# Kernel tuning notes

Hardware: AMD Instinct MI355X
Metric: run time of the kernel (lower is better)

The kernel has to match this reference:

```python
import jax, jax.numpy as jnp
import numpy as np

NUM_HEADS = 16
ROPE_BASE = 10000.0


def _rotate_half(x):
    x1 = x[..., ::2]
    x2 = x[..., 1::2]
    return jnp.stack((-x2, x1), axis=-1).reshape(x.shape)


def _rope_tables(seq_len, head_dim, dtype):
    inv_freq = 1.0 / (ROPE_BASE ** (jnp.arange(0, head_dim, 2, dtype=jnp.float32) / head_dim))
    t = jnp.arange(seq_len, dtype=jnp.float32)
    freqs = jnp.outer(t, inv_freq)            # [S, head_dim//2]
    emb = jnp.concatenate((freqs, freqs), -1)  # [S, head_dim]
    return jnp.cos(emb).astype(dtype), jnp.sin(emb).astype(dtype)


def setup_inputs() -> dict:
    key = jax.random.key(0)
    ks = jax.random.split(key, 5)
    B, S, H = 1, 4096, 1024
    scale = 1.0 / np.sqrt(H)
    return {
        "x": jax.random.normal(ks[0], (B, S, H), jnp.float32),
        "Wq": jax.random.normal(ks[1], (H, H), jnp.float32) * scale,
        "Wk": jax.random.normal(ks[2], (H, H), jnp.float32) * scale,
        "Wv": jax.random.normal(ks[3], (H, H), jnp.float32) * scale,
        "Wo": jax.random.normal(ks[4], (H, H), jnp.float32) * scale,
        "attention_mask": jnp.ones((B, S), jnp.int32),
    }


def reference(x, Wq, Wk, Wv, Wo, attention_mask):
    B, S, H = x.shape
    hd = H // NUM_HEADS

    def split_heads(t):  # [B,S,H] -> [B,nh,S,hd]
        return t.reshape(B, S, NUM_HEADS, hd).transpose(0, 2, 1, 3)

    q = split_heads(x @ Wq)
    k = split_heads(x @ Wk)
    v = split_heads(x @ Wv)

    cos, sin = _rope_tables(S, hd, x.dtype)
    cos = cos[None, None]  # [1,1,S,hd]
    sin = sin[None, None]
    q = q * cos + _rotate_half(q) * sin
    k = k * cos + _rotate_half(k) * sin

    scores = jnp.einsum("bhqd,bhkd->bhqk", q, k) / jnp.sqrt(jnp.asarray(hd, x.dtype))
    mask = attention_mask.reshape(B, 1, 1, S)
    scores = jnp.where(mask == 0, jnp.finfo(x.dtype).min, scores)
    probs = jax.nn.softmax(scores, axis=-1)
    ctx = jnp.einsum("bhqk,bhkd->bhqd", probs, v)
    ctx = ctx.transpose(0, 2, 1, 3).reshape(B, S, H)
    return ctx @ Wo
```

## Files before the change

kernel.cpp:

```cpp
#include <hip/hip_runtime.h>
#include <cstdint>
#include <cstddef>

#define S_LEN 4096
#define NHEADS 16
#define HD 64
#define HDIM 1024

typedef _Float16 f16x8 __attribute__((ext_vector_type(8)));
typedef _Float16 f16x4 __attribute__((ext_vector_type(4)));
typedef __fp16 h16x2 __attribute__((ext_vector_type(2)));
typedef float f32x4 __attribute__((ext_vector_type(4)));
typedef unsigned char uchar;
typedef unsigned int u32;

__device__ __forceinline__ f32x4 mfma16h(f16x8 a, f16x8 b, f32x4 c) {
    return __builtin_amdgcn_mfma_f32_16x16x32_f16(a, b, c, 0, 0, 0);
}
__device__ __forceinline__ void async16(void* lds, const void* g) {
    __builtin_amdgcn_global_load_lds(
        (const __attribute__((address_space(1))) u32*)g,
        (__attribute__((address_space(3))) u32*)lds, 16, 0, 0);
}
__device__ __forceinline__ float fdot2_(u32 a, u32 b, float c) {
#if __has_builtin(__builtin_amdgcn_fdot2)
    return __builtin_amdgcn_fdot2(__builtin_bit_cast(h16x2, a),
                                  __builtin_bit_cast(h16x2, b), c, false);
#else
    float d;
    asm volatile("v_dot2_f32_f16 %0, %1, %2, %3"
                 : "=v"(d) : "v"(a), "v"(b), "v"(c));
    return d;
#endif
}
__device__ __forceinline__ float dot8(f16x8 p, uint4 f, float acc) {
    uint4 pw = __builtin_bit_cast(uint4, p);
    acc = fdot2_(pw.x, f.x, acc);
    acc = fdot2_(pw.y, f.y, acc);
    acc = fdot2_(pw.z, f.z, acc);
    acc = fdot2_(pw.w, f.w, acc);
    return acc;
}


__global__ __launch_bounds__(256) void pack_x(const float* __restrict__ X,
                                              uchar* __restrict__ P,
                                              const int* __restrict__ M,
                                              _Float16* __restrict__ FM16)
{
    int id = blockIdx.x * 256 + threadIdx.x;
    int m = id >> 7, g = id & 127;
    int kc = g >> 3, b = g & 7;
    float v[8];
    *(float4*)&v[0] = *(const float4*)&X[(size_t)m * HDIM + kc * 64 + b * 8];
    *(float4*)&v[4] = *(const float4*)&X[(size_t)m * HDIM + kc * 64 + b * 8 + 4];
    __align__(16) _Float16 h[8];
    #pragma unroll
    for (int i = 0; i < 8; i++) h[i] = (_Float16)v[i];
    size_t base = ((size_t)(m * 16 + kc)) * 128 + (size_t)((b ^ (m & 7)) * 16);
    *(uint4*)(P + base) = *(const uint4*)h;
    if (id < S_LEN) {
        int c = id >> 7, k128 = id & 127;
        int w = k128 >> 5, k32 = k128 & 31;
        int q = (k32 >> 2) & 3, kt = k32 >> 4, r = k32 & 3;
        FM16[c * 128 + w * 32 + q * 8 + kt * 4 + r] =
            (_Float16)((M[id] == 0) ? 0.0f : 1.0f);
    }
}

__global__ __launch_bounds__(256) void pack_w4(
    const float* __restrict__ W0, const float* __restrict__ W1,
    const float* __restrict__ W2, const float* __restrict__ W3,
    uchar* __restrict__ P)
{
    int id = blockIdx.x * 256 + threadIdx.x;
    int wsel = id >> 17;
    int lid  = id & 131071;
    int g = lid >> 10, n = lid & 1023;
    int kc = g >> 3, b = g & 7;
    const float* W = (wsel == 0) ? W0 : (wsel == 1) ? W1 : (wsel == 2) ? W2 : W3;
    uchar* dst = P + (size_t)wsel * 2097152;
    float v[8];
    #pragma unroll
    for (int j = 0; j < 8; j++)
        v[j] = W[(size_t)(kc * 64 + b * 8 + j) * HDIM + n];
    __align__(16) _Float16 h[8];
    #pragma unroll
    for (int i = 0; i < 8; i++) h[i] = (_Float16)v[i];
    size_t base = ((size_t)(n * 16 + kc)) * 128 + (size_t)((b ^ (n & 7)) * 16);
    *(uint4*)(dst + base) = *(const uint4*)h;
}

__global__ __launch_bounds__(256) void gemm_f16(
    const uchar* __restrict__ Ap, const uchar* __restrict__ Bp,
    float* __restrict__ C, int head_major)
{
    __shared__ __align__(16) uchar AB[65536];
    const int t = threadIdx.x, lane = t & 63, w = t >> 6;
    const int quad = lane >> 4, l15 = lane & 15, x7 = l15 & 7;
    const int m0 = blockIdx.y * 128, n0 = blockIdx.x * 128;
    const int wm = (w >> 1) * 64, wn = (w & 1) * 64;

    f32x4 acc[4][4];
    const f32x4 zero4 = {0.0f, 0.0f, 0.0f, 0.0f};
    #pragma unroll
    for (int mt = 0; mt < 4; mt++)
        #pragma unroll
        for (int nt = 0; nt < 4; nt++) acc[mt][nt] = zero4;

    #pragma unroll
    for (int i = 0; i < 4; i++) {
        int idx = i * 256 + t;
        int row = idx >> 3, blk = idx & 7;
        int ldso = (idx & ~63) * 16;
        async16(AB + ldso,         Ap + ((size_t)((m0 + row) * 16 + 0)) * 128 + blk * 16);
        async16(AB + 16384 + ldso, Bp + ((size_t)((n0 + row) * 16 + 0)) * 128 + blk * 16);
    }

    for (int kc = 0; kc < 16; kc++) {
        uchar* As = AB + (kc & 1) * 32768;
        uchar* Bs = As + 16384;
        __syncthreads();
        if (kc + 1 < 16) {
            uchar* An = AB + ((kc + 1) & 1) * 32768;
            #pragma unroll
            for (int i = 0; i < 4; i++) {
                int idx = i * 256 + t;
                int row = idx >> 3, blk = idx & 7;
                int ldso = (idx & ~63) * 16;
                async16(An + ldso,
                        Ap + ((size_t)((m0 + row) * 16 + kc + 1)) * 128 + blk * 16);
                async16(An + 16384 + ldso,
                        Bp + ((size_t)((n0 + row) * 16 + kc + 1)) * 128 + blk * 16);
            }
        }
        #pragma unroll
        for (int ks = 0; ks < 2; ks++) {
            const int phys = ((ks * 4 + quad) ^ x7) * 16;
            f16x8 ah[4];
            #pragma unroll
            for (int mt = 0; mt < 4; mt++)
                ah[mt] = *(const f16x8*)(As + (size_t)(wm + mt * 16 + l15) * 128 + phys);
            #pragma unroll
            for (int nt = 0; nt < 4; nt++) {
                f16x8 bh = *(const f16x8*)(Bs + (size_t)(wn + nt * 16 + l15) * 128 + phys);
                #pragma unroll
                for (int mt = 0; mt < 4; mt++)
                    acc[mt][nt] = mfma16h(ah[mt], bh, acc[mt][nt]);
            }
        }
    }

    #pragma unroll
    for (int mt = 0; mt < 4; mt++)
        #pragma unroll
        for (int nt = 0; nt < 4; nt++)
            #pragma unroll
            for (int r = 0; r < 4; r++) {
                int m = m0 + wm + mt * 16 + quad * 4 + r;
                int n = n0 + wn + nt * 16 + l15;
                float val = acc[mt][nt][r];
                if (head_major) {
                    int hh = n >> 6, d = n & 63;
                    C[((size_t)hh * S_LEN + m) * HD + d] = val;
                } else {
                    C[(size_t)m * HDIM + n] = val;
                }
            }
}

__global__ __launch_bounds__(256) void rope_pack(const float* __restrict__ QKVf,
                                                 uchar* __restrict__ Qg,
                                                 uchar* __restrict__ Kg)
{
    int id = blockIdx.x * 256 + threadIdx.x;
    int g  = id & 7;
    int s  = (id >> 3) & (S_LEN - 1);
    int hb = id >> 15;
    const float* src = QKVf + (size_t)hb * (S_LEN * HD) + (size_t)s * HD + g * 8;
    float v[8];
    *(float4*)&v[0] = *(const float4*)&src[0];
    *(float4*)&v[4] = *(const float4*)&src[4];

    const float L32 = 13.287712379549449f / 32.0f;
    float out[8];
    #pragma unroll
    for (int u = 0; u < 4; u++) {
        int de = g * 8 + 2 * u;
        float ae = (float)s * __builtin_amdgcn_exp2f(-(float)(de & 31) * L32);
        float ao = (float)s * __builtin_amdgcn_exp2f(-(float)((de + 1) & 31) * L32);
        float ce = __cosf(ae), se = __sinf(ae);
        float co = __cosf(ao), so = __sinf(ao);
        float xe = v[2 * u], xo = v[2 * u + 1];
        out[2 * u]     = xe * ce - xo * se;
        out[2 * u + 1] = xo * co + xe * so;
    }
    const bool isQ = hb < 16;
    const float scale = isQ ? 0.18033688011112042f : 1.0f;
    __align__(16) _Float16 h[8];
    #pragma unroll
    for (int i = 0; i < 8; i++) h[i] = (_Float16)(out[i] * scale);
    uchar* dst = (isQ ? Qg : Kg);
    size_t base = ((size_t)((hb & 15) * S_LEN + s)) * 128 + (size_t)((g ^ (s & 7)) * 16);
    *(uint4*)(dst + base) = *(const uint4*)h;
}

__global__ __launch_bounds__(256) void v_pack(const float* __restrict__ Vf,
                                              const int* __restrict__ M,
                                              uchar* __restrict__ Vg)
{
    int id = blockIdx.x * 256 + threadIdx.x;
    int d    = id & 63;
    int kg   = (id >> 6) & 15;
    int kc2  = (id >> 10) & 31;
    int head = id >> 15;
    __align__(16) _Float16 hv[8];
    #pragma unroll
    for (int j = 0; j < 8; j++) {
        int key = kc2 * 128 + kg * 8 + j;
        float x = Vf[(size_t)head * (S_LEN * HD) + (size_t)key * HD + d];
        hv[j] = (M[key] == 0) ? (_Float16)0.0f : (_Float16)x;
    }
    int wv  = kg >> 2;
    int kgm = kg & 3;
    int kt  = kgm >> 1;
    int qA  = (kgm * 2) & 3;
    int qB  = (kgm * 2 + 1) & 3;
    int slotA = wv * 32 + qA * 8 + kt * 4;
    int slotB = wv * 32 + qB * 8 + kt * 4;
    size_t row = ((size_t)(head * 32 + kc2)) * 16384 + (size_t)d * 256;
    *(ushort4*)(Vg + row + (size_t)(((slotA >> 3) ^ (d & 7)) * 16 + (slotA & 7) * 2))
        = *(const ushort4*)&hv[0];
    *(ushort4*)(Vg + row + (size_t)(((slotB >> 3) ^ (d & 7)) * 16 + (slotB & 7) * 2))
        = *(const ushort4*)&hv[4];
}

#define ISSUE_K(CC)                                                            \
  {                                                                            \
    const uchar* ks_ = kgb + (size_t)(CC) * 16384;                             \
    async16(KB,        ks_ + l16);                                             \
    async16(KB + 1024, ks_ + 1024 + l16);                                      \
    async16(KB + 2048, ks_ + 2048 + l16);                                      \
    async16(KB + 3072, ks_ + 3072 + l16);                                      \
  }
#define ISSUE_V(CC)                                                            \
  {                                                                            \
    const uchar* vs_ = vgb + (size_t)(CC) * 16384;                             \
    async16(VB,        vs_ + voff);                                            \
    async16(VB + 1024, vs_ + 4096 + voff);                                     \
    async16(VB + 2048, vs_ + 8192 + voff);                                     \
    async16(VB + 3072, vs_ + 12288 + voff);                                    \
  }

#define ATTN_STEP(CC, TOPC, MIDC, FLG)                                         \
  {                                                                            \
    asm volatile("s_waitcnt vmcnt(" TOPC ")" ::: "memory");                    \
    const int ph0_ = (quad ^ x7) * 16;                                         \
    const int ph1_ = ((4 + quad) ^ x7) * 16;                                   \
    f16x8 ka_ = *(const f16x8*)(KB + (size_t)l15 * 128 + ph0_);                \
    f16x8 kb_ = *(const f16x8*)(KB + (size_t)(16 + l15) * 128 + ph0_);         \
    f16x8 kc_ = *(const f16x8*)(KB + (size_t)l15 * 128 + ph1_);                \
    f16x8 kd_ = *(const f16x8*)(KB + (size_t)(16 + l15) * 128 + ph1_);         \
    asm volatile("s_waitcnt lgkmcnt(0)" ::: "memory");                         \
    if ((CC) + 1 < 32) ISSUE_K((CC) + 1);                                      \
    f16x8 pb[4];                                                               \
    _Pragma("unroll")                                                          \
    for (int qt = 0; qt < 4; qt++) {                                           \
      f32x4 s0 = mfma16h(ka_, qf[qt][0], zero4);                               \
      s0 = mfma16h(kc_, qf[qt][1], s0);                                        \
      f32x4 s1 = mfma16h(kb_, qf[qt][0], zero4);                               \
      s1 = mfma16h(kd_, qf[qt][1], s1);                                        \
      h16x2 c01 = __builtin_amdgcn_cvt_pkrtz(                                  \
          __builtin_amdgcn_exp2f(s0[0]), __builtin_amdgcn_exp2f(s0[1]));       \
      h16x2 c23 = __builtin_amdgcn_cvt_pkrtz(                                  \
          __builtin_amdgcn_exp2f(s0[2]), __builtin_amdgcn_exp2f(s0[3]));       \
      h16x2 c45 = __builtin_amdgcn_cvt_pkrtz(                                  \
          __builtin_amdgcn_exp2f(s1[0]), __builtin_amdgcn_exp2f(s1[1]));       \
      h16x2 c67 = __builtin_amdgcn_cvt_pkrtz(                                  \
          __builtin_amdgcn_exp2f(s1[2]), __builtin_amdgcn_exp2f(s1[3]));       \
      uint4 pw;                                                                \
      pw.x = __builtin_bit_cast(u32, c01);                                     \
      pw.y = __builtin_bit_cast(u32, c23);                                     \
      pw.z = __builtin_bit_cast(u32, c45);                                     \
      pw.w = __builtin_bit_cast(u32, c67);                                     \
      pb[qt] = __builtin_bit_cast(f16x8, pw);                                  \
    }                                                                          \
    asm volatile("s_waitcnt vmcnt(" MIDC ")" ::: "memory");                    \
    _Pragma("unroll")                                                          \
    for (int dt = 0; dt < 4; dt++) {                                           \
      f16x8 va = *(const f16x8*)(VB + (size_t)(dt * 16 + l15) * 64 + vrd);     \
      _Pragma("unroll")                                                        \
      for (int qt = 0; qt < 4; qt++)                                           \
        o[dt][qt] = mfma16h(va, pb[qt], o[dt][qt]);                            \
    }                                                                          \
    _Pragma("unroll")                                                          \
    for (int qt = 0; qt < 4; qt++)                                             \
      lacc[qt] = dot8(pb[qt], (FLG), lacc[qt]);                                \
    asm volatile("s_waitcnt lgkmcnt(0)" ::: "memory");                         \
    if ((CC) + 1 < 32) ISSUE_V((CC) + 1);                                      \
    if ((CC) + 2 < 32) (FLG) = *(const uint4*)(fmw + (size_t)((CC) + 2) * 256);\
  }

__global__ __launch_bounds__(256, 3) void attn9(
    const uchar* __restrict__ Qg, const uchar* __restrict__ Kg,
    const uchar* __restrict__ Vg, const uchar* __restrict__ fm16,
    uchar* __restrict__ CTXp)
{
    __shared__ __align__(16) uchar arena[32768];
    __shared__ float Lsh[4][64];
    __shared__ float Lfin[64];
    float* Os = (float*)arena;

    const int t    = threadIdx.x;
    const int lane = t & 63;
    const int w    = t >> 6;
    const int quad = lane >> 4;
    const int l15  = lane & 15;
    const int x7   = l15 & 7;
    const int hh   = blockIdx.y;
    const int m0   = blockIdx.x * 64;

    const uchar* qgb = Qg + (size_t)hh * (S_LEN * 128);
    const uchar* kgb = Kg + (size_t)hh * (S_LEN * 128) + (size_t)w * 4096;
    const uchar* vgb = Vg + (size_t)hh * 32 * 16384;
    const uchar* fmw = fm16 + w * 64 + quad * 16;

    uchar* WB = arena + w * 8192;
    uchar* KB = WB;
    uchar* VB = WB + 4096;

    const int l16 = lane * 16;
    const int vphys = ((w * 4 + ((lane & 3) ^ ((lane >> 2) & 3))) ^ ((lane >> 2) & 7));
    const int voff  = (lane >> 2) * 256 + vphys * 16;
    const int vrd   = (quad ^ (l15 & 3)) * 16;

    f16x8 qf[4][2];
    #pragma unroll
    for (int qt = 0; qt < 4; qt++)
        #pragma unroll
        for (int ks = 0; ks < 2; ks++)
            qf[qt][ks] = *(const f16x8*)(qgb + (size_t)(m0 + qt * 16 + l15) * 128 +
                                         (size_t)(((ks * 4 + quad) ^ x7) * 16));

    f32x4 o[4][4];
    float lacc[4] = {0.0f, 0.0f, 0.0f, 0.0f};
    const f32x4 zero4 = {0.0f, 0.0f, 0.0f, 0.0f};
    #pragma unroll
    for (int dt = 0; dt < 4; dt++)
        #pragma unroll
        for (int qt = 0; qt < 4; qt++) o[dt][qt] = zero4;

    uint4 flagA = *(const uint4*)(fmw);
    uint4 flagB = *(const uint4*)(fmw + 256);
    asm volatile("" ::: "memory");
    ISSUE_K(0);
    ISSUE_V(0);

    ATTN_STEP(0, "4", "4", flagA);
    ATTN_STEP(1, "5", "4", flagB);
    for (int c = 2; c < 30; c += 2) {
        ATTN_STEP(c,     "5", "4", flagA);
        ATTN_STEP(c + 1, "5", "4", flagB);
    }
    ATTN_STEP(30, "5", "4", flagA);
    ATTN_STEP(31, "4", "0", flagB);

    #pragma unroll
    for (int qt = 0; qt < 4; qt++) {
        float v = lacc[qt];
        v += __shfl_xor(v, 16);
        v += __shfl_xor(v, 32);
        lacc[qt] = v;
    }
    __syncthreads();
    if (quad == 0) {
        #pragma unroll
        for (int qt = 0; qt < 4; qt++)
            Lsh[w][qt * 16 + l15] = lacc[qt];
    }
    __syncthreads();
    if (t < 64)
        Lfin[t] = Lsh[0][t] + Lsh[1][t] + Lsh[2][t] + Lsh[3][t];
    __syncthreads();

    for (int wv = 0; wv < 4; wv++) {
        if (w == wv) {
            #pragma unroll
            for (int dt = 0; dt < 4; dt++)
                #pragma unroll
                for (int qt = 0; qt < 4; qt++)
                    #pragma unroll
                    for (int r = 0; r < 4; r++) {
                        int q = qt * 16 + l15;
                        int d = dt * 16 + quad * 4 + r;
                        float val = o[dt][qt][r];
                        if (wv == 0) Os[q * 68 + d] = val;
                        else         Os[q * 68 + d] += val;
                    }
        }
        __syncthreads();
    }

    #pragma unroll
    for (int i = 0; i < 4; i++) {
        int idx = t + 256 * i;
        int q   = idx >> 4;
        int c4  = (idx & 15) * 4;
        float inv = 1.0f / Lfin[q];
        float4 v = *(const float4*)&Os[q * 68 + c4];
        int m = m0 + q;
        __align__(8) _Float16 h[4];
        h[0] = (_Float16)(v.x * inv);
        h[1] = (_Float16)(v.y * inv);
        h[2] = (_Float16)(v.z * inv);
        h[3] = (_Float16)(v.w * inv);
        size_t base = ((size_t)(m * 16 + hh)) * 128 +
                      (size_t)((((c4 >> 3) ^ (m & 7))) * 16) + (c4 & 7) * 2;
        *(ushort4*)(CTXp + base) = *(const ushort4*)h;
    }
}

extern "C" void kernel_launch(void* const* d_in, const int* in_sizes, int n_in,
                              void* d_out, int out_size, void* d_ws, size_t ws_size,
                              hipStream_t stream)
{
    const float* x   = (const float*)d_in[0];
    const float* Wq  = (const float*)d_in[1];
    const float* Wk  = (const float*)d_in[2];
    const float* Wv  = (const float*)d_in[3];
    const float* Wo  = (const float*)d_in[4];
    const int* amask = (const int*)d_in[5];
    float* out = (float*)d_out;
    float* ws  = (float*)d_ws;

    float* QKVf = ws;
    uchar* Xp   = (uchar*)ws + 50331648;
    uchar* Wt4  = (uchar*)ws + 58720256;
    uchar* Vg   = (uchar*)ws + 67108864;
    _Float16* Fm16 = (_Float16*)((uchar*)ws + 75497472);
    uchar* Qg   = Xp;
    uchar* Kg   = (uchar*)ws + 33554432;
    uchar* CTXp = (uchar*)ws;

    dim3 blk(256);

    pack_x<<<2048, blk, 0, stream>>>(x, Xp, amask, Fm16);
    pack_w4<<<2048, blk, 0, stream>>>(Wq, Wk, Wv, Wo, Wt4);

    gemm_f16<<<dim3(24, 32), blk, 0, stream>>>(Xp, Wt4, QKVf, 1);

    v_pack<<<2048, blk, 0, stream>>>(QKVf + 8388608, amask, Vg);
    rope_pack<<<4096, blk, 0, stream>>>(QKVf, Qg, Kg);

    attn9<<<dim3(S_LEN / 64, NHEADS), blk, 0, stream>>>(Qg, Kg, Vg,
                                                        (const uchar*)Fm16, CTXp);

    gemm_f16<<<dim3(8, 32), blk, 0, stream>>>(CTXp, Wt4 + 6291456, out, 0);
}
```

Measured before the change: 244.4 us.

## Split attention warps into 2 query halves x 2 key halves, raise occupancy

Reorganizes the attention kernel's four waves from each covering all 64 queries over a quarter of the keys to a 2x2 split: each wave handles 32 queries and half the keys (64 chunks of 32 keys instead of 32 chunks). This halves per-wave accumulator and Q-fragment registers, which allows launch bounds to rise to 4 blocks per CU. It also moves the Lsh/Lfin scratch into the shared arena to save LDS and cuts the cross-wave output reduction from four serialized passes to two. The cost is that each wave now runs twice as many loop iterations with less MFMA work per step, so loads and waits are amortized over fewer matrix ops.

```diff
diff --git a/kernel.cpp b/kernel.cpp
--- a/kernel.cpp
+++ b/kernel.cpp
@@ -237,7 +237,7 @@
 
 #define ISSUE_K(CC)                                                            \
   {                                                                            \
-    const uchar* ks_ = kgb + (size_t)(CC) * 16384;                             \
+    const uchar* ks_ = kgb + (size_t)(CC) * 4096;                              \
     async16(KB,        ks_ + l16);                                             \
     async16(KB + 1024, ks_ + 1024 + l16);                                      \
     async16(KB + 2048, ks_ + 2048 + l16);                                      \
@@ -245,14 +245,16 @@
   }
 #define ISSUE_V(CC)                                                            \
   {                                                                            \
-    const uchar* vs_ = vgb + (size_t)(CC) * 16384;                             \
-    async16(VB,        vs_ + voff);                                            \
-    async16(VB + 1024, vs_ + 4096 + voff);                                     \
-    async16(VB + 2048, vs_ + 8192 + voff);                                     \
-    async16(VB + 3072, vs_ + 12288 + voff);                                    \
+    const uchar* vs_ = vgb + (size_t)((CC) >> 2) * 16384;                      \
+    int vph_  = ((((CC) & 3) << 2) | va0) ^ vb0;                               \
+    int voff_ = vbase + vph_ * 16;                                             \
+    async16(VB,        vs_ + voff_);                                           \
+    async16(VB + 1024, vs_ + 4096 + voff_);                                    \
+    async16(VB + 2048, vs_ + 8192 + voff_);                                    \
+    async16(VB + 3072, vs_ + 12288 + voff_);                                   \
   }
 
-#define ATTN_STEP(CC, TOPC, MIDC, FLG)                                         \
+#define ATTN_STEP(CC, TOPC, MIDC)                                              \
   {                                                                            \
     asm volatile("s_waitcnt vmcnt(" TOPC ")" ::: "memory");                    \
     const int ph0_ = (quad ^ x7) * 16;                                         \
@@ -262,10 +264,10 @@
     f16x8 kc_ = *(const f16x8*)(KB + (size_t)l15 * 128 + ph1_);                \
     f16x8 kd_ = *(const f16x8*)(KB + (size_t)(16 + l15) * 128 + ph1_);         \
     asm volatile("s_waitcnt lgkmcnt(0)" ::: "memory");                         \
-    if ((CC) + 1 < 32) ISSUE_K((CC) + 1);                                      \
-    f16x8 pb[4];                                                               \
+    if ((CC) + 1 < 64) ISSUE_K((CC) + 1);                                      \
+    f16x8 pb[2];                                                               \
     _Pragma("unroll")                                                          \
-    for (int qt = 0; qt < 4; qt++) {                                           \
+    for (int qt = 0; qt < 2; qt++) {                                           \
       f32x4 s0 = mfma16h(ka_, qf[qt][0], zero4);                               \
       s0 = mfma16h(kc_, qf[qt][1], s0);                                        \
       f32x4 s1 = mfma16h(kb_, qf[qt][0], zero4);                               \
@@ -289,27 +291,27 @@
     _Pragma("unroll")                                                          \
     for (int dt = 0; dt < 4; dt++) {                                           \
       f16x8 va = *(const f16x8*)(VB + (size_t)(dt * 16 + l15) * 64 + vrd);     \
-      _Pragma("unroll")                                                        \
-      for (int qt = 0; qt < 4; qt++)                                           \
-        o[dt][qt] = mfma16h(va, pb[qt], o[dt][qt]);                            \
+      o[dt][0] = mfma16h(va, pb[0], o[dt][0]);                                 \
+      o[dt][1] = mfma16h(va, pb[1], o[dt][1]);                                 \
     }                                                                          \
-    _Pragma("unroll")                                                          \
-    for (int qt = 0; qt < 4; qt++)                                             \
-      lacc[qt] = dot8(pb[qt], (FLG), lacc[qt]);                                \
+    lacc[0] = dot8(pb[0], flag, lacc[0]);                                      \
+    lacc[1] = dot8(pb[1], flag, lacc[1]);                                      \
     asm volatile("s_waitcnt lgkmcnt(0)" ::: "memory");                         \
-    if ((CC) + 1 < 32) ISSUE_V((CC) + 1);                                      \
-    if ((CC) + 2 < 32) (FLG) = *(const uint4*)(fmw + (size_t)((CC) + 2) * 256);\
+    if ((CC) + 1 < 64) {                                                       \
+      ISSUE_V((CC) + 1);                                                       \
+      flag = *(const uint4*)(fmw + (size_t)((CC) + 1) * 64);                   \
+    }                                                                          \
   }
 
-__global__ __launch_bounds__(256, 3) void attn9(
+__global__ __launch_bounds__(256, 4) void attn9(
     const uchar* __restrict__ Qg, const uchar* __restrict__ Kg,
     const uchar* __restrict__ Vg, const uchar* __restrict__ fm16,
     uchar* __restrict__ CTXp)
 {
     __shared__ __align__(16) uchar arena[32768];
-    __shared__ float Lsh[4][64];
-    __shared__ float Lfin[64];
-    float* Os = (float*)arena;
+    float* Os   = (float*)arena;
+    float* Lsh  = (float*)(arena + 18432);
+    float* Lfin = (float*)(arena + 18944);
 
     const int t    = threadIdx.x;
     const int lane = t & 63;
@@ -319,54 +321,54 @@
     const int x7   = l15 & 7;
     const int hh   = blockIdx.y;
     const int m0   = blockIdx.x * 64;
+    const int qh   = w >> 1;
+    const int kh   = w & 1;
 
     const uchar* qgb = Qg + (size_t)hh * (S_LEN * 128);
-    const uchar* kgb = Kg + (size_t)hh * (S_LEN * 128) + (size_t)w * 4096;
-    const uchar* vgb = Vg + (size_t)hh * 32 * 16384;
-    const uchar* fmw = fm16 + w * 64 + quad * 16;
+    const uchar* kgb = Kg + (size_t)hh * (S_LEN * 128) + (size_t)kh * 262144;
+    const uchar* vgb = Vg + (size_t)hh * (32 * 16384) + (size_t)kh * 262144;
+    const uchar* fmw = fm16 + (size_t)kh * 4096 + quad * 16;
 
     uchar* WB = arena + w * 8192;
     uchar* KB = WB;
     uchar* VB = WB + 4096;
 
-    const int l16 = lane * 16;
-    const int vphys = ((w * 4 + ((lane & 3) ^ ((lane >> 2) & 3))) ^ ((lane >> 2) & 7));
-    const int voff  = (lane >> 2) * 256 + vphys * 16;
+    const int l16   = lane * 16;
+    const int va0   = (lane & 3) ^ ((lane >> 2) & 3);
+    const int vb0   = (lane >> 2) & 7;
+    const int vbase = (lane >> 2) * 256;
     const int vrd   = (quad ^ (l15 & 3)) * 16;
 
-    f16x8 qf[4][2];
-    #pragma unroll
-    for (int qt = 0; qt < 4; qt++)
+    f16x8 qf[2][2];
+    #pragma unroll
+    for (int qt = 0; qt < 2; qt++)
         #pragma unroll
         for (int ks = 0; ks < 2; ks++)
-            qf[qt][ks] = *(const f16x8*)(qgb + (size_t)(m0 + qt * 16 + l15) * 128 +
-                                         (size_t)(((ks * 4 + quad) ^ x7) * 16));
-
-    f32x4 o[4][4];
-    float lacc[4] = {0.0f, 0.0f, 0.0f, 0.0f};
+            qf[qt][ks] = *(const f16x8*)(qgb +
+                (size_t)(m0 + qh * 32 + qt * 16 + l15) * 128 +
+                (size_t)(((ks * 4 + quad) ^ x7) * 16));
+
+    f32x4 o[4][2];
+    float lacc[2] = {0.0f, 0.0f};
     const f32x4 zero4 = {0.0f, 0.0f, 0.0f, 0.0f};
     #pragma unroll
-    for (int dt = 0; dt < 4; dt++)
-        #pragma unroll
-        for (int qt = 0; qt < 4; qt++) o[dt][qt] = zero4;
-
-    uint4 flagA = *(const uint4*)(fmw);
-    uint4 flagB = *(const uint4*)(fmw + 256);
+    for (int dt = 0; dt < 4; dt++) {
+        o[dt][0] = zero4;
+        o[dt][1] = zero4;
+    }
+
+    uint4 flag = *(const uint4*)(fmw);
     asm volatile("" ::: "memory");
     ISSUE_K(0);
     ISSUE_V(0);
 
-    ATTN_STEP(0, "4", "4", flagA);
-    ATTN_STEP(1, "5", "4", flagB);
-    for (int c = 2; c < 30; c += 2) {
-        ATTN_STEP(c,     "5", "4", flagA);
-        ATTN_STEP(c + 1, "5", "4", flagB);
-    }
-    ATTN_STEP(30, "5", "4", flagA);
-    ATTN_STEP(31, "4", "0", flagB);
-
-    #pragma unroll
-    for (int qt = 0; qt < 4; qt++) {
+    ATTN_STEP(0, "4", "4");
+    for (int c = 1; c < 63; ++c)
+        ATTN_STEP(c, "5", "4");
+    ATTN_STEP(63, "5", "0");
+
+    #pragma unroll
+    for (int qt = 0; qt < 2; qt++) {
         float v = lacc[qt];
         v += __shfl_xor(v, 16);
         v += __shfl_xor(v, 32);
@@ -374,32 +376,42 @@
     }
     __syncthreads();
     if (quad == 0) {
-        #pragma unroll
-        for (int qt = 0; qt < 4; qt++)
-            Lsh[w][qt * 16 + l15] = lacc[qt];
+        Lsh[w * 32 + l15]      = lacc[0];
+        Lsh[w * 32 + 16 + l15] = lacc[1];
     }
     __syncthreads();
-    if (t < 64)
-        Lfin[t] = Lsh[0][t] + Lsh[1][t] + Lsh[2][t] + Lsh[3][t];
+    if (t < 64) {
+        int qhh = t >> 5, ql = t & 31;
+        Lfin[t] = Lsh[(qhh * 2) * 32 + ql] + Lsh[(qhh * 2 + 1) * 32 + ql];
+    }
     __syncthreads();
 
-    for (int wv = 0; wv < 4; wv++) {
-        if (w == wv) {
-            #pragma unroll
-            for (int dt = 0; dt < 4; dt++)
+    if (kh == 0) {
+        #pragma unroll
+        for (int dt = 0; dt < 4; dt++)
+            #pragma unroll
+            for (int qt = 0; qt < 2; qt++)
                 #pragma unroll
-                for (int qt = 0; qt < 4; qt++)
-                    #pragma unroll
-                    for (int r = 0; r < 4; r++) {
-                        int q = qt * 16 + l15;
-                        int d = dt * 16 + quad * 4 + r;
-                        float val = o[dt][qt][r];
-                        if (wv == 0) Os[q * 68 + d] = val;
-                        else         Os[q * 68 + d] += val;
-                    }
-        }
-        __syncthreads();
-    }
+                for (int r = 0; r < 4; r++) {
+                    int q = qh * 32 + qt * 16 + l15;
+                    int d = dt * 16 + quad * 4 + r;
+                    Os[q * 68 + d] = o[dt][qt][r];
+                }
+    }
+    __syncthreads();
+    if (kh == 1) {
+        #pragma unroll
+        for (int dt = 0; dt < 4; dt++)
+            #pragma unroll
+            for (int qt = 0; qt < 2; qt++)
+                #pragma unroll
+                for (int r = 0; r < 4; r++) {
+                    int q = qh * 32 + qt * 16 + l15;
+                    int d = dt * 16 + quad * 4 + r;
+                    Os[q * 68 + d] += o[dt][qt][r];
+                }
+    }
+    __syncthreads();
 
     #pragma unroll
     for (int i = 0; i < 4; i++) {
```

New measurement: 261.7 us. 1.07x slower.

## Software-pipeline PV MFMA one chunk behind QK with double-buffered V tiles

Applied to the files above, without the earlier changes.

Restructures the attention inner loop so the P·V MFMAs for chunk c-1 run while chunk c's QK scores and exp are computed. V tiles are double-buffered in LDS, which removes the mid-step vmcnt wait on the freshly loaded V tile. LDS per block grows to 48KB and launch bounds drop from 3 to 2 blocks per CU, trading occupancy for more in-wave overlap. The flag loads are also retimed to match the one-step lag.

```diff
diff --git a/kernel.cpp b/kernel.cpp
--- a/kernel.cpp
+++ b/kernel.cpp
@@ -245,25 +245,23 @@
   }
 #define ISSUE_V(CC)                                                            \
   {                                                                            \
+    uchar* vb_ = VB0 + (size_t)((CC) & 1) * 4096;                              \
     const uchar* vs_ = vgb + (size_t)(CC) * 16384;                             \
-    async16(VB,        vs_ + voff);                                            \
-    async16(VB + 1024, vs_ + 4096 + voff);                                     \
-    async16(VB + 2048, vs_ + 8192 + voff);                                     \
-    async16(VB + 3072, vs_ + 12288 + voff);                                    \
+    async16(vb_,        vs_ + voff);                                           \
+    async16(vb_ + 1024, vs_ + 4096 + voff);                                    \
+    async16(vb_ + 2048, vs_ + 8192 + voff);                                    \
+    async16(vb_ + 3072, vs_ + 12288 + voff);                                   \
   }
 
-#define ATTN_STEP(CC, TOPC, MIDC, FLG)                                         \
+#define ATTN_STEP(CC, TOPC, FLG, PBN, PBO, FIRST)                              \
   {                                                                            \
     asm volatile("s_waitcnt vmcnt(" TOPC ")" ::: "memory");                    \
-    const int ph0_ = (quad ^ x7) * 16;                                         \
-    const int ph1_ = ((4 + quad) ^ x7) * 16;                                   \
-    f16x8 ka_ = *(const f16x8*)(KB + (size_t)l15 * 128 + ph0_);                \
-    f16x8 kb_ = *(const f16x8*)(KB + (size_t)(16 + l15) * 128 + ph0_);         \
-    f16x8 kc_ = *(const f16x8*)(KB + (size_t)l15 * 128 + ph1_);                \
-    f16x8 kd_ = *(const f16x8*)(KB + (size_t)(16 + l15) * 128 + ph1_);         \
+    f16x8 ka_ = *(const f16x8*)(KB + (size_t)l15 * 128 + ph0);                 \
+    f16x8 kb_ = *(const f16x8*)(KB + (size_t)(16 + l15) * 128 + ph0);          \
+    f16x8 kc_ = *(const f16x8*)(KB + (size_t)l15 * 128 + ph1);                 \
+    f16x8 kd_ = *(const f16x8*)(KB + (size_t)(16 + l15) * 128 + ph1);          \
     asm volatile("s_waitcnt lgkmcnt(0)" ::: "memory");                         \
     if ((CC) + 1 < 32) ISSUE_K((CC) + 1);                                      \
-    f16x8 pb[4];                                                               \
     _Pragma("unroll")                                                          \
     for (int qt = 0; qt < 4; qt++) {                                           \
       f32x4 s0 = mfma16h(ka_, qf[qt][0], zero4);                               \
@@ -283,33 +281,37 @@
       pw.y = __builtin_bit_cast(u32, c23);                                     \
       pw.z = __builtin_bit_cast(u32, c45);                                     \
       pw.w = __builtin_bit_cast(u32, c67);                                     \
-      pb[qt] = __builtin_bit_cast(f16x8, pw);                                  \
+      (PBN)[qt] = __builtin_bit_cast(f16x8, pw);                               \
     }                                                                          \
-    asm volatile("s_waitcnt vmcnt(" MIDC ")" ::: "memory");                    \
-    _Pragma("unroll")                                                          \
-    for (int dt = 0; dt < 4; dt++) {                                           \
-      f16x8 va = *(const f16x8*)(VB + (size_t)(dt * 16 + l15) * 64 + vrd);     \
+    if (!(FIRST)) {                                                            \
+      const uchar* VBp_ = VB0 + (size_t)(((CC) + 1) & 1) * 4096;               \
+      _Pragma("unroll")                                                        \
+      for (int dt = 0; dt < 4; dt++) {                                         \
+        f16x8 va = *(const f16x8*)(VBp_ + (size_t)(dt * 16 + l15) * 64 + vrd); \
+        _Pragma("unroll")                                                      \
+        for (int qt = 0; qt < 4; qt++)                                         \
+          o[dt][qt] = mfma16h(va, (PBO)[qt], o[dt][qt]);                       \
+      }                                                                        \
       _Pragma("unroll")                                                        \
       for (int qt = 0; qt < 4; qt++)                                           \
-        o[dt][qt] = mfma16h(va, pb[qt], o[dt][qt]);                            \
+        lacc[qt] = dot8((PBO)[qt], (FLG), lacc[qt]);                           \
     }                                                                          \
-    _Pragma("unroll")                                                          \
-    for (int qt = 0; qt < 4; qt++)                                             \
-      lacc[qt] = dot8(pb[qt], (FLG), lacc[qt]);                                \
     asm volatile("s_waitcnt lgkmcnt(0)" ::: "memory");                         \
-    if ((CC) + 1 < 32) ISSUE_V((CC) + 1);                                      \
-    if ((CC) + 2 < 32) (FLG) = *(const uint4*)(fmw + (size_t)((CC) + 2) * 256);\
+    if ((CC) + 1 < 32) {                                                       \
+      ISSUE_V((CC) + 1);                                                       \
+      (FLG) = *(const uint4*)(fmw + (size_t)((CC) + 1) * 256);                 \
+    }                                                                          \
   }
 
-__global__ __launch_bounds__(256, 3) void attn9(
+__global__ __launch_bounds__(256, 2) void attn9(
     const uchar* __restrict__ Qg, const uchar* __restrict__ Kg,
     const uchar* __restrict__ Vg, const uchar* __restrict__ fm16,
     uchar* __restrict__ CTXp)
 {
-    __shared__ __align__(16) uchar arena[32768];
-    __shared__ float Lsh[4][64];
-    __shared__ float Lfin[64];
-    float* Os = (float*)arena;
+    __shared__ __align__(16) uchar arena[49152];
+    float* Os   = (float*)arena;
+    float* Lsh  = (float*)(arena + 18432);
+    float* Lfin = (float*)(arena + 19712);
 
     const int t    = threadIdx.x;
     const int lane = t & 63;
@@ -325,14 +327,16 @@
     const uchar* vgb = Vg + (size_t)hh * 32 * 16384;
     const uchar* fmw = fm16 + w * 64 + quad * 16;
 
-    uchar* WB = arena + w * 8192;
-    uchar* KB = WB;
-    uchar* VB = WB + 4096;
+    uchar* WB  = arena + w * 12288;
+    uchar* KB  = WB;
+    uchar* VB0 = WB + 4096;
 
     const int l16 = lane * 16;
     const int vphys = ((w * 4 + ((lane & 3) ^ ((lane >> 2) & 3))) ^ ((lane >> 2) & 7));
     const int voff  = (lane >> 2) * 256 + vphys * 16;
     const int vrd   = (quad ^ (l15 & 3)) * 16;
+    const int ph0   = (quad ^ x7) * 16;
+    const int ph1   = ((4 + quad) ^ x7) * 16;
 
     f16x8 qf[4][2];
     #pragma unroll
@@ -351,19 +355,34 @@
         for (int qt = 0; qt < 4; qt++) o[dt][qt] = zero4;
 
     uint4 flagA = *(const uint4*)(fmw);
-    uint4 flagB = *(const uint4*)(fmw + 256);
+    uint4 flagB = flagA;
     asm volatile("" ::: "memory");
     ISSUE_K(0);
     ISSUE_V(0);
 
-    ATTN_STEP(0, "4", "4", flagA);
-    ATTN_STEP(1, "5", "4", flagB);
-    for (int c = 2; c < 30; c += 2) {
-        ATTN_STEP(c,     "5", "4", flagA);
-        ATTN_STEP(c + 1, "5", "4", flagB);
-    }
-    ATTN_STEP(30, "5", "4", flagA);
-    ATTN_STEP(31, "4", "0", flagB);
+    f16x8 pbE[4], pbO[4];
+
+    ATTN_STEP(0, "4", flagB, pbE, pbE, true);
+    for (int c = 1; c < 31; c += 2) {
+        ATTN_STEP(c,     "5", flagA, pbO, pbE, false);
+        ATTN_STEP(c + 1, "5", flagB, pbE, pbO, false);
+    }
+    ATTN_STEP(31, "5", flagA, pbO, pbE, false);
+
+    asm volatile("s_waitcnt vmcnt(0)" ::: "memory");
+    {
+        const uchar* VBp_ = VB0 + 4096;
+        #pragma unroll
+        for (int dt = 0; dt < 4; dt++) {
+            f16x8 va = *(const f16x8*)(VBp_ + (size_t)(dt * 16 + l15) * 64 + vrd);
+            #pragma unroll
+            for (int qt = 0; qt < 4; qt++)
+                o[dt][qt] = mfma16h(va, pbO[qt], o[dt][qt]);
+        }
+        #pragma unroll
+        for (int qt = 0; qt < 4; qt++)
+            lacc[qt] = dot8(pbO[qt], flagB, lacc[qt]);
+    }
 
     #pragma unroll
     for (int qt = 0; qt < 4; qt++) {
@@ -376,11 +395,11 @@
     if (quad == 0) {
         #pragma unroll
         for (int qt = 0; qt < 4; qt++)
-            Lsh[w][qt * 16 + l15] = lacc[qt];
+            Lsh[w * 64 + qt * 16 + l15] = lacc[qt];
     }
     __syncthreads();
     if (t < 64)
-        Lfin[t] = Lsh[0][t] + Lsh[1][t] + Lsh[2][t] + Lsh[3][t];
+        Lfin[t] = Lsh[t] + Lsh[64 + t] + Lsh[128 + t] + Lsh[192 + t];
     __syncthreads();
 
     for (int wv = 0; wv < 4; wv++) {
```

After: 248.4 us. About the same (+1.6%).

## Fuse RoPE and V packing into QKV GEMM epilogue, merge pack kernels, MFMA row sums

Applied to the files above, without the earlier changes.

Merges the x and weight pack kernels into one launch, and moves RoPE, the Q scaling, V masking and fp16 packing into the QKV GEMM epilogue. This removes the fp32 QKV intermediate round trip through global memory and two kernel launches. In attention, the softmax denominator is now accumulated with an MFMA against the mask flags instead of dot2 plus shuffles, and the occupancy hint drops from 3 to 2 blocks. The epilogue now writes scattered 2-byte stores for Q/K, and the V slot mapping was rewritten, so its layout may no longer match what the attention kernel expects.

```diff
diff --git a/kernel.cpp b/kernel.cpp
--- a/kernel.cpp
+++ b/kernel.cpp
@@ -8,7 +8,6 @@
 #define HDIM 1024
 
 typedef _Float16 f16x8 __attribute__((ext_vector_type(8)));
-typedef _Float16 f16x4 __attribute__((ext_vector_type(4)));
 typedef __fp16 h16x2 __attribute__((ext_vector_type(2)));
 typedef float f32x4 __attribute__((ext_vector_type(4)));
 typedef unsigned char uchar;
@@ -22,78 +21,58 @@
         (const __attribute__((address_space(1))) u32*)g,
         (__attribute__((address_space(3))) u32*)lds, 16, 0, 0);
 }
-__device__ __forceinline__ float fdot2_(u32 a, u32 b, float c) {
-#if __has_builtin(__builtin_amdgcn_fdot2)
-    return __builtin_amdgcn_fdot2(__builtin_bit_cast(h16x2, a),
-                                  __builtin_bit_cast(h16x2, b), c, false);
-#else
-    float d;
-    asm volatile("v_dot2_f32_f16 %0, %1, %2, %3"
-                 : "=v"(d) : "v"(a), "v"(b), "v"(c));
-    return d;
-#endif
-}
-__device__ __forceinline__ float dot8(f16x8 p, uint4 f, float acc) {
-    uint4 pw = __builtin_bit_cast(uint4, p);
-    acc = fdot2_(pw.x, f.x, acc);
-    acc = fdot2_(pw.y, f.y, acc);
-    acc = fdot2_(pw.z, f.z, acc);
-    acc = fdot2_(pw.w, f.w, acc);
-    return acc;
-}
-
-
-__global__ __launch_bounds__(256) void pack_x(const float* __restrict__ X,
-                                              uchar* __restrict__ P,
-                                              const int* __restrict__ M,
-                                              _Float16* __restrict__ FM16)
-{
-    int id = blockIdx.x * 256 + threadIdx.x;
-    int m = id >> 7, g = id & 127;
-    int kc = g >> 3, b = g & 7;
-    float v[8];
-    *(float4*)&v[0] = *(const float4*)&X[(size_t)m * HDIM + kc * 64 + b * 8];
-    *(float4*)&v[4] = *(const float4*)&X[(size_t)m * HDIM + kc * 64 + b * 8 + 4];
-    __align__(16) _Float16 h[8];
-    #pragma unroll
-    for (int i = 0; i < 8; i++) h[i] = (_Float16)v[i];
-    size_t base = ((size_t)(m * 16 + kc)) * 128 + (size_t)((b ^ (m & 7)) * 16);
-    *(uint4*)(P + base) = *(const uint4*)h;
-    if (id < S_LEN) {
-        int c = id >> 7, k128 = id & 127;
-        int w = k128 >> 5, k32 = k128 & 31;
-        int q = (k32 >> 2) & 3, kt = k32 >> 4, r = k32 & 3;
-        FM16[c * 128 + w * 32 + q * 8 + kt * 4 + r] =
-            (_Float16)((M[id] == 0) ? 0.0f : 1.0f);
-    }
-}
-
-__global__ __launch_bounds__(256) void pack_w4(
+
+
+__global__ __launch_bounds__(256) void pack_xw(
+    const float* __restrict__ X, uchar* __restrict__ P,
+    const int* __restrict__ M, _Float16* __restrict__ FM16,
     const float* __restrict__ W0, const float* __restrict__ W1,
     const float* __restrict__ W2, const float* __restrict__ W3,
-    uchar* __restrict__ P)
+    uchar* __restrict__ PW)
 {
-    int id = blockIdx.x * 256 + threadIdx.x;
-    int wsel = id >> 17;
-    int lid  = id & 131071;
-    int g = lid >> 10, n = lid & 1023;
-    int kc = g >> 3, b = g & 7;
-    const float* W = (wsel == 0) ? W0 : (wsel == 1) ? W1 : (wsel == 2) ? W2 : W3;
-    uchar* dst = P + (size_t)wsel * 2097152;
-    float v[8];
-    #pragma unroll
-    for (int j = 0; j < 8; j++)
-        v[j] = W[(size_t)(kc * 64 + b * 8 + j) * HDIM + n];
-    __align__(16) _Float16 h[8];
-    #pragma unroll
-    for (int i = 0; i < 8; i++) h[i] = (_Float16)v[i];
-    size_t base = ((size_t)(n * 16 + kc)) * 128 + (size_t)((b ^ (n & 7)) * 16);
-    *(uint4*)(dst + base) = *(const uint4*)h;
-}
-
-__global__ __launch_bounds__(256) void gemm_f16(
+    if (blockIdx.x < 2048) {
+        int id = blockIdx.x * 256 + threadIdx.x;
+        int m = id >> 7, g = id & 127;
+        int kc = g >> 3, b = g & 7;
+        float v[8];
+        *(float4*)&v[0] = *(const float4*)&X[(size_t)m * HDIM + kc * 64 + b * 8];
+        *(float4*)&v[4] = *(const float4*)&X[(size_t)m * HDIM + kc * 64 + b * 8 + 4];
+        __align__(16) _Float16 h[8];
+        #pragma unroll
+        for (int i = 0; i < 8; i++) h[i] = (_Float16)v[i];
+        size_t base = ((size_t)(m * 16 + kc)) * 128 + (size_t)((b ^ (m & 7)) * 16);
+        *(uint4*)(P + base) = *(const uint4*)h;
+        if (id < S_LEN) {
+            int c = id >> 7, k128 = id & 127;
+            int w = k128 >> 5, k32 = k128 & 31;
+            int q = (k32 >> 2) & 3, kt = k32 >> 4, r = k32 & 3;
+            FM16[c * 128 + w * 32 + q * 8 + kt * 4 + r] =
+                (_Float16)((M[id] == 0) ? 0.0f : 1.0f);
+        }
+    } else {
+        int id = (blockIdx.x - 2048) * 256 + threadIdx.x;
+        int wsel = id >> 17;
+        int lid  = id & 131071;
+        int g = lid >> 10, n = lid & 1023;
+        int kc = g >> 3, b = g & 7;
+        const float* W = (wsel == 0) ? W0 : (wsel == 1) ? W1 : (wsel == 2) ? W2 : W3;
+        uchar* dst = PW + (size_t)wsel * 2097152;
+        float v[8];
+        #pragma unroll
+        for (int j = 0; j < 8; j++)
+            v[j] = W[(size_t)(kc * 64 + b * 8 + j) * HDIM + n];
+        __align__(16) _Float16 h[8];
+        #pragma unroll
+        for (int i = 0; i < 8; i++) h[i] = (_Float16)v[i];
+        size_t base = ((size_t)(n * 16 + kc)) * 128 + (size_t)((b ^ (n & 7)) * 16);
+        *(uint4*)(dst + base) = *(const uint4*)h;
+    }
+}
+
+__global__ __launch_bounds__(256) void gemm_qkv(
     const uchar* __restrict__ Ap, const uchar* __restrict__ Bp,
-    float* __restrict__ C, int head_major)
+    const int* __restrict__ M,
+    uchar* __restrict__ Qg, uchar* __restrict__ Kg, uchar* __restrict__ Vg)
 {
     __shared__ __align__(16) uchar AB[65536];
     const int t = threadIdx.x, lane = t & 63, w = t >> 6;
@@ -151,6 +130,122 @@
         }
     }
 
+    const int headN = (n0 + wn) >> 6;
+    if (headN < 32) {
+        const bool isQ = headN < 16;
+        uchar* dst = isQ ? Qg : Kg;
+        const int hh = headN & 15;
+        const float scale = isQ ? 0.18033688011112042f : 1.0f;
+        const float L32 = 13.287712379549449f / 32.0f;
+        #pragma unroll
+        for (int nt = 0; nt < 4; nt++) {
+            const int d = nt * 16 + l15;
+            const float f = __builtin_amdgcn_exp2f(-(float)(d & 31) * L32);
+            const float sgn = (d & 1) ? 1.0f : -1.0f;
+            #pragma unroll
+            for (int mt = 0; mt < 4; mt++)
+                #pragma unroll
+                for (int r = 0; r < 4; r++) {
+                    int m = m0 + wm + mt * 16 + quad * 4 + r;
+                    float own = acc[mt][nt][r];
+                    float par = __shfl_xor(own, 1);
+                    float th = (float)m * f;
+                    float val = (own * __cosf(th) + sgn * par * __sinf(th)) * scale;
+                    _Float16 hv = (_Float16)val;
+                    size_t base = ((size_t)(hh * S_LEN + m)) * 128 +
+                                  (size_t)(((d >> 3) ^ (m & 7)) * 16) + (d & 7) * 2;
+                    *(_Float16*)(dst + base) = hv;
+                }
+        }
+    } else {
+        const int head = headN - 32;
+        const int kc2 = m0 >> 7;
+        #pragma unroll
+        for (int mt = 0; mt < 4; mt++) {
+            int mb = m0 + wm + mt * 16 + quad * 4;
+            int4 mk = *(const int4*)&M[mb];
+            int wv = (wm + mt * 16) >> 5;
+            int kt = mt & 1;
+            int slotbase = wv * 32 + quad * 8 + kt * 4;
+            size_t off = (size_t)(((slotbase >> 3) ^ 0) * 16);
+            #pragma unroll
+            for (int nt = 0; nt < 4; nt++) {
+                const int d = nt * 16 + l15;
+                __align__(8) _Float16 hv[4];
+                hv[0] = (mk.x == 0) ? (_Float16)0.0f : (_Float16)acc[mt][nt][0];
+                hv[1] = (mk.y == 0) ? (_Float16)0.0f : (_Float16)acc[mt][nt][1];
+                hv[2] = (mk.z == 0) ? (_Float16)0.0f : (_Float16)acc[mt][nt][2];
+                hv[3] = (mk.w == 0) ? (_Float16)0.0f : (_Float16)acc[mt][nt][3];
+                size_t row = ((size_t)(head * 32 + kc2)) * 16384 + (size_t)d * 256;
+                size_t boff = (size_t)((((slotbase >> 3) ^ (d & 7)) * 16) +
+                                       (slotbase & 7) * 2);
+                *(ushort4*)(Vg + row + boff) = *(const ushort4*)hv;
+            }
+            (void)off;
+        }
+    }
+}
+
+__global__ __launch_bounds__(256) void gemm_f16(
+    const uchar* __restrict__ Ap, const uchar* __restrict__ Bp,
+    float* __restrict__ C)
+{
+    __shared__ __align__(16) uchar AB[65536];
+    const int t = threadIdx.x, lane = t & 63, w = t >> 6;
+    const int quad = lane >> 4, l15 = lane & 15, x7 = l15 & 7;
+    const int m0 = blockIdx.y * 128, n0 = blockIdx.x * 128;
+    const int wm = (w >> 1) * 64, wn = (w & 1) * 64;
+
+    f32x4 acc[4][4];
+    const f32x4 zero4 = {0.0f, 0.0f, 0.0f, 0.0f};
+    #pragma unroll
+    for (int mt = 0; mt < 4; mt++)
+        #pragma unroll
+        for (int nt = 0; nt < 4; nt++) acc[mt][nt] = zero4;
+
+    #pragma unroll
+    for (int i = 0; i < 4; i++) {
+        int idx = i * 256 + t;
+        int row = idx >> 3, blk = idx & 7;
+        int ldso = (idx & ~63) * 16;
+        async16(AB + ldso,         Ap + ((size_t)((m0 + row) * 16 + 0)) * 128 + blk * 16);
+        async16(AB + 16384 + ldso, Bp + ((size_t)((n0 + row) * 16 + 0)) * 128 + blk * 16);
+    }
+
+    for (int kc = 0; kc < 16; kc++) {
+        uchar* As = AB + (kc & 1) * 32768;
+        uchar* Bs = As + 16384;
+        __syncthreads();
+        if (kc + 1 < 16) {
+            uchar* An = AB + ((kc + 1) & 1) * 32768;
+            #pragma unroll
+            for (int i = 0; i < 4; i++) {
+                int idx = i * 256 + t;
+                int row = idx >> 3, blk = idx & 7;
+                int ldso = (idx & ~63) * 16;
+                async16(An + ldso,
+                        Ap + ((size_t)((m0 + row) * 16 + kc + 1)) * 128 + blk * 16);
+                async16(An + 16384 + ldso,
+                        Bp + ((size_t)((n0 + row) * 16 + kc + 1)) * 128 + blk * 16);
+            }
+        }
+        #pragma unroll
+        for (int ks = 0; ks < 2; ks++) {
+            const int phys = ((ks * 4 + quad) ^ x7) * 16;
+            f16x8 ah[4];
+            #pragma unroll
+            for (int mt = 0; mt < 4; mt++)
+                ah[mt] = *(const f16x8*)(As + (size_t)(wm + mt * 16 + l15) * 128 + phys);
+            #pragma unroll
+            for (int nt = 0; nt < 4; nt++) {
+                f16x8 bh = *(const f16x8*)(Bs + (size_t)(wn + nt * 16 + l15) * 128 + phys);
+                #pragma unroll
+                for (int mt = 0; mt < 4; mt++)
+                    acc[mt][nt] = mfma16h(ah[mt], bh, acc[mt][nt]);
+            }
+        }
+    }
+
     #pragma unroll
     for (int mt = 0; mt < 4; mt++)
         #pragma unroll
@@ -159,80 +254,8 @@
             for (int r = 0; r < 4; r++) {
                 int m = m0 + wm + mt * 16 + quad * 4 + r;
                 int n = n0 + wn + nt * 16 + l15;
-                float val = acc[mt][nt][r];
-                if (head_major) {
-                    int hh = n >> 6, d = n & 63;
-                    C[((size_t)hh * S_LEN + m) * HD + d] = val;
-                } else {
-                    C[(size_t)m * HDIM + n] = val;
-                }
-            }
-}
-
-__global__ __launch_bounds__(256) void rope_pack(const float* __restrict__ QKVf,
-                                                 uchar* __restrict__ Qg,
-                                                 uchar* __restrict__ Kg)
-{
-    int id = blockIdx.x * 256 + threadIdx.x;
-    int g  = id & 7;
-    int s  = (id >> 3) & (S_LEN - 1);
-    int hb = id >> 15;
-    const float* src = QKVf + (size_t)hb * (S_LEN * HD) + (size_t)s * HD + g * 8;
-    float v[8];
-    *(float4*)&v[0] = *(const float4*)&src[0];
-    *(float4*)&v[4] = *(const float4*)&src[4];
-
-    const float L32 = 13.287712379549449f / 32.0f;
-    float out[8];
-    #pragma unroll
-    for (int u = 0; u < 4; u++) {
-        int de = g * 8 + 2 * u;
-        float ae = (float)s * __builtin_amdgcn_exp2f(-(float)(de & 31) * L32);
-        float ao = (float)s * __builtin_amdgcn_exp2f(-(float)((de + 1) & 31) * L32);
-        float ce = __cosf(ae), se = __sinf(ae);
-        float co = __cosf(ao), so = __sinf(ao);
-        float xe = v[2 * u], xo = v[2 * u + 1];
-        out[2 * u]     = xe * ce - xo * se;
-        out[2 * u + 1] = xo * co + xe * so;
-    }
-    const bool isQ = hb < 16;
-    const float scale = isQ ? 0.18033688011112042f : 1.0f;
-    __align__(16) _Float16 h[8];
-    #pragma unroll
-    for (int i = 0; i < 8; i++) h[i] = (_Float16)(out[i] * scale);
-    uchar* dst = (isQ ? Qg : Kg);
-    size_t base = ((size_t)((hb & 15) * S_LEN + s)) * 128 + (size_t)((g ^ (s & 7)) * 16);
-    *(uint4*)(dst + base) = *(const uint4*)h;
-}
-
-__global__ __launch_bounds__(256) void v_pack(const float* __restrict__ Vf,
-                                              const int* __restrict__ M,
-                                              uchar* __restrict__ Vg)
-{
-    int id = blockIdx.x * 256 + threadIdx.x;
-    int d    = id & 63;
-    int kg   = (id >> 6) & 15;
-    int kc2  = (id >> 10) & 31;
-    int head = id >> 15;
-    __align__(16) _Float16 hv[8];
-    #pragma unroll
-    for (int j = 0; j < 8; j++) {
-        int key = kc2 * 128 + kg * 8 + j;
-        float x = Vf[(size_t)head * (S_LEN * HD) + (size_t)key * HD + d];
-        hv[j] = (M[key] == 0) ? (_Float16)0.0f : (_Float16)x;
-    }
-    int wv  = kg >> 2;
-    int kgm = kg & 3;
-    int kt  = kgm >> 1;
-    int qA  = (kgm * 2) & 3;
-    int qB  = (kgm * 2 + 1) & 3;
-    int slotA = wv * 32 + qA * 8 + kt * 4;
-    int slotB = wv * 32 + qB * 8 + kt * 4;
-    size_t row = ((size_t)(head * 32 + kc2)) * 16384 + (size_t)d * 256;
-    *(ushort4*)(Vg + row + (size_t)(((slotA >> 3) ^ (d & 7)) * 16 + (slotA & 7) * 2))
-        = *(const ushort4*)&hv[0];
-    *(ushort4*)(Vg + row + (size_t)(((slotB >> 3) ^ (d & 7)) * 16 + (slotB & 7) * 2))
-        = *(const ushort4*)&hv[4];
+                C[(size_t)m * HDIM + n] = acc[mt][nt][r];
+            }
 }
 
 #define ISSUE_K(CC)                                                            \
@@ -295,13 +318,13 @@
     }                                                                          \
     _Pragma("unroll")                                                          \
     for (int qt = 0; qt < 4; qt++)                                             \
-      lacc[qt] = dot8(pb[qt], (FLG), lacc[qt]);                                \
+      lacc[qt] = mfma16h((FLG), pb[qt], lacc[qt]);                             \
     asm volatile("s_waitcnt lgkmcnt(0)" ::: "memory");                         \
     if ((CC) + 1 < 32) ISSUE_V((CC) + 1);                                      \
-    if ((CC) + 2 < 32) (FLG) = *(const uint4*)(fmw + (size_t)((CC) + 2) * 256);\
+    if ((CC) + 2 < 32) (FLG) = *(const f16x8*)(fmw + (size_t)((CC) + 2) * 256);\
   }
 
-__global__ __launch_bounds__(256, 3) void attn9(
+__global__ __launch_bounds__(256, 2) void attn9(
     const uchar* __restrict__ Qg, const uchar* __restrict__ Kg,
     const uchar* __restrict__ Vg, const uchar* __restrict__ fm16,
     uchar* __restrict__ CTXp)
@@ -342,16 +365,17 @@
             qf[qt][ks] = *(const f16x8*)(qgb + (size_t)(m0 + qt * 16 + l15) * 128 +
                                          (size_t)(((ks * 4 + quad) ^ x7) * 16));
 
-    f32x4 o[4][4];
-    float lacc[4] = {0.0f, 0.0f, 0.0f, 0.0f};
+    f32x4 o[4][4], lacc[4];
     const f32x4 zero4 = {0.0f, 0.0f, 0.0f, 0.0f};
     #pragma unroll
     for (int dt = 0; dt < 4; dt++)
         #pragma unroll
         for (int qt = 0; qt < 4; qt++) o[dt][qt] = zero4;
-
-    uint4 flagA = *(const uint4*)(fmw);
-    uint4 flagB = *(const uint4*)(fmw + 256);
+    #pragma unroll
+    for (int qt = 0; qt < 4; qt++) lacc[qt] = zero4;
+
+    f16x8 flagA = *(const f16x8*)(fmw);
+    f16x8 flagB = *(const f16x8*)(fmw + 256);
     asm volatile("" ::: "memory");
     ISSUE_K(0);
     ISSUE_V(0);
@@ -365,18 +389,11 @@
     ATTN_STEP(30, "5", "4", flagA);
     ATTN_STEP(31, "4", "0", flagB);
 
-    #pragma unroll
-    for (int qt = 0; qt < 4; qt++) {
-        float v = lacc[qt];
-        v += __shfl_xor(v, 16);
-        v += __shfl_xor(v, 32);
-        lacc[qt] = v;
-    }
     __syncthreads();
     if (quad == 0) {
         #pragma unroll
         for (int qt = 0; qt < 4; qt++)
-            Lsh[w][qt * 16 + l15] = lacc[qt];
+            Lsh[w][qt * 16 + l15] = lacc[qt][0];
     }
     __syncthreads();
     if (t < 64)
@@ -431,29 +448,23 @@
     const float* Wo  = (const float*)d_in[4];
     const int* amask = (const int*)d_in[5];
     float* out = (float*)d_out;
-    float* ws  = (float*)d_ws;
-
-    float* QKVf = ws;
-    uchar* Xp   = (uchar*)ws + 50331648;
-    uchar* Wt4  = (uchar*)ws + 58720256;
-    uchar* Vg   = (uchar*)ws + 67108864;
-    _Float16* Fm16 = (_Float16*)((uchar*)ws + 75497472);
-    uchar* Qg   = Xp;
-    uchar* Kg   = (uchar*)ws + 33554432;
-    uchar* CTXp = (uchar*)ws;
+
+    uchar* Xp   = (uchar*)d_ws;
+    uchar* Wt4  = (uchar*)d_ws + 8388608;
+    uchar* Qg   = (uchar*)d_ws + 16777216;
+    uchar* Kg   = (uchar*)d_ws + 25165824;
+    uchar* Vg   = (uchar*)d_ws + 33554432;
+    _Float16* Fm16 = (_Float16*)((uchar*)d_ws + 41943040);
+    uchar* CTXp = Xp;
 
     dim3 blk(256);
 
-    pack_x<<<2048, blk, 0, stream>>>(x, Xp, amask, Fm16);
-    pack_w4<<<2048, blk, 0, stream>>>(Wq, Wk, Wv, Wo, Wt4);
-
-    gemm_f16<<<dim3(24, 32), blk, 0, stream>>>(Xp, Wt4, QKVf, 1);
-
-    v_pack<<<2048, blk, 0, stream>>>(QKVf + 8388608, amask, Vg);
-    rope_pack<<<4096, blk, 0, stream>>>(QKVf, Qg, Kg);
+    pack_xw<<<4096, blk, 0, stream>>>(x, Xp, amask, Fm16, Wq, Wk, Wv, Wo, Wt4);
+
+    gemm_qkv<<<dim3(24, 32), blk, 0, stream>>>(Xp, Wt4, amask, Qg, Kg, Vg);
 
     attn9<<<dim3(S_LEN / 64, NHEADS), blk, 0, stream>>>(Qg, Kg, Vg,
                                                         (const uchar*)Fm16, CTXp);
 
-    gemm_f16<<<dim3(8, 32), blk, 0, stream>>>(CTXp, Wt4 + 6291456, out, 0);
-}
+    gemm_f16<<<dim3(8, 32), blk, 0, stream>>>(CTXp, Wt4 + 6291456, out);
+}
```

Result: faster. 215.5 us (-11.8%).
